# Kernel optimization log

Hardware: AMD Instinct MI355X
Metric: run time of the kernel (lower is better)

The kernel has to match this reference:

```python
import jax, jax.numpy as jnp
import numpy as np

B, S, V, P = 16, 100, 50000, 45
WE, PE, H = 100, 50, 400
H2 = 2 * H  # bilstm output size


def _lstm(x, Wih, Whh, b):
    """Unidirectional LSTM over time. x: [B,S,D] -> h: [B,S,H]. PyTorch gate order i,f,g,o."""
    Hs = Whh.shape[1]
    def step(carry, xt):
        h, c = carry
        g = xt @ Wih.T + h @ Whh.T + b
        i, f, gg, o = jnp.split(g, 4, axis=-1)
        c = jax.nn.sigmoid(f) * c + jax.nn.sigmoid(i) * jnp.tanh(gg)
        h = jax.nn.sigmoid(o) * jnp.tanh(c)
        return (h, c), h
    Bn = x.shape[0]
    init = (jnp.zeros((Bn, Hs), x.dtype), jnp.zeros((Bn, Hs), x.dtype))
    _, hs = jax.lax.scan(step, init, jnp.swapaxes(x, 0, 1))
    return jnp.swapaxes(hs, 0, 1)


def _bilstm_layer(x, Wf_ih, Wf_hh, bf, Wb_ih, Wb_hh, bb):
    hf = _lstm(x, Wf_ih, Wf_hh, bf)
    hb = _lstm(x[:, ::-1, :], Wb_ih, Wb_hh, bb)[:, ::-1, :]
    return jnp.concatenate([hf, hb], axis=-1)


def setup_inputs() -> dict:
    key = jax.random.key(0)
    ks = jax.random.split(key, 24)
    def n(k, shape, s=0.1):
        return jax.random.normal(k, shape, jnp.float32) * s
    inp = {
        "input_tokens": jax.random.randint(ks[0], (B, S), 0, V),
        "input_pos": jax.random.randint(ks[1], (B, S), 0, P),
        "input_head": jax.random.randint(ks[2], (B, S), 0, S),
        "word_W": n(ks[3], (V, WE)),
        "pos_W": n(ks[4], (P, PE)),
        "l0f_Wih": n(ks[5], (4 * H, WE + PE)), "l0f_Whh": n(ks[6], (4 * H, H)), "l0f_b": n(ks[7], (4 * H,)),
        "l0b_Wih": n(ks[8], (4 * H, WE + PE)), "l0b_Whh": n(ks[9], (4 * H, H)), "l0b_b": n(ks[10], (4 * H,)),
        "l1f_Wih": n(ks[11], (4 * H, H2)), "l1f_Whh": n(ks[12], (4 * H, H)), "l1f_b": n(ks[13], (4 * H,)),
        "l1b_Wih": n(ks[14], (4 * H, H2)), "l1b_Whh": n(ks[15], (4 * H, H)), "l1b_b": n(ks[16], (4 * H,)),
        "ua_W": n(ks[17], (H2, H2)), "ua_b": n(ks[18], (H2,)),
        "wa_W": n(ks[19], (H2, H2)), "wa_b": n(ks[20], (H2,)),
        "va_W": n(ks[21], (H2,)),
    }
    return inp


def reference(input_tokens, input_pos, input_head, word_W, pos_W,
              l0f_Wih, l0f_Whh, l0f_b, l0b_Wih, l0b_Whh, l0b_b,
              l1f_Wih, l1f_Whh, l1f_b, l1b_Wih, l1b_Whh, l1b_b,
              ua_W, ua_b, wa_W, wa_b, va_W):
    # embeddings (dropout is identity at eval)
    x = jnp.concatenate([word_W[input_tokens], pos_W[input_pos]], axis=-1)  # [B,S,150]
    h1 = _bilstm_layer(x, l0f_Wih, l0f_Whh, l0f_b, l0b_Wih, l0b_Whh, l0b_b)   # [B,S,H2]
    out = _bilstm_layer(h1, l1f_Wih, l1f_Whh, l1f_b, l1b_Wih, l1b_Whh, l1b_b)  # [B,S,H2]

    # batched additive biaffine scoring for targets i = 1..S-1 over all source positions j
    ua = out @ ua_W.T + ua_b  # u_a(source)  [B,S,H2]
    wa = out @ wa_W.T + wa_b  # w_a(target)  [B,S,H2]
    # g[b,t,j] = v_a . tanh(ua[b,j] + wa[b,t+1])
    g = jnp.einsum('btjh,h->btj', jnp.tanh(ua[:, None, :, :] + wa[:, 1:, None, :]), va_W)  # [B,S-1,S]
    # mask: output[:, j, 0] == output[:, i, 0]  (masks self, matching torch's output.eq(target)[:,:,0])
    mask = out[:, 1:, 0][:, :, None] == out[:, :, 0][:, None, :]  # [B,S-1,S]
    g = jnp.where(mask, -10000.0, g)
    logp = jax.nn.log_softmax(g, axis=2)  # log_softmax over source positions (torch dim=1)

    # loss: sum over i of NLLLoss(mean over batch, ignore_index=-1)
    gold = input_head[:, 1:]  # [B,S-1]
    valid = (gold != -1)
    nll = -jnp.take_along_axis(logp, jnp.clip(gold, 0, S - 1)[:, :, None], axis=2)[..., 0]
    nll = nll * valid.astype(logp.dtype)
    denom = jnp.maximum(valid.sum(axis=0), 1).astype(logp.dtype)
    loss = jnp.sum(nll.sum(axis=0) / denom)

    parent_prob_table = jnp.exp(logp)  # [B,S-1,S]
    preds = jnp.argmax(parent_prob_table, axis=2)  # [B,S-1]
    return (loss, preds, parent_prob_table)
```

## Files before the change

### kernel.cpp

```cpp
#include <hip/hip_runtime.h>

#define BB 16
#define SS 100
#define HH 400
#define H2 800
#define G4 1600
#define DIN0 150
#define KP0 160

#define OFF_GF   240000ULL
#define OFF_GB   2800000ULL
#define OFF_H1   5360000ULL
#define OFF_OUT2 6640000ULL
#define OFF_SC   7920000ULL
#define OFF_NLL  8078400ULL
#define OFF_EXH  8081600ULL
#define EX_U16_PER_PLANE 1331200ULL

#define PAD_X0   0ULL
#define PAD_WF   256000ULL
#define PAD_WB   512000ULL

typedef _Float16 f16x8 __attribute__((ext_vector_type(8)));
typedef float    f32x4 __attribute__((ext_vector_type(4)));
typedef unsigned long long u64x2 __attribute__((ext_vector_type(2)));

static __device__ __forceinline__ unsigned chkp(unsigned long long q) {
    return ((unsigned)q == 0xFFFFFFFFu) | ((unsigned)(q >> 32) == 0xFFFFFFFFu);
}
static __device__ __forceinline__ unsigned long long sanq(unsigned long long q) {
    if ((unsigned)q == 0xFFFFFFFFu)         q &= 0xFFFFFFFF00000000ull;
    if ((unsigned)(q >> 32) == 0xFFFFFFFFu) q &= 0x00000000FFFFFFFFull;
    return q;
}

__global__ __launch_bounds__(256) void embed_pad_kernel(
    const int* __restrict__ tok, const int* __restrict__ pos,
    const float* __restrict__ wW, const float* __restrict__ pW,
    const float* __restrict__ Wf, const float* __restrict__ Wb,
    float* __restrict__ stage)
{
    int idx = blockIdx.x * 256 + threadIdx.x;
    if (idx >= 3 * 1600 * KP0) return;
    int which = idx / (1600 * KP0);
    int rem = idx % (1600 * KP0);
    int r = rem / KP0, k = rem % KP0;
    float v = 0.f;
    if (which == 0) {
        if (k < 100)       v = wW[tok[r] * 100 + k];
        else if (k < 150)  v = pW[pos[r] * 50 + (k - 100)];
        stage[PAD_X0 + (size_t)r * KP0 + k] = v;
    } else if (which == 1) {
        if (k < DIN0) v = Wf[r * DIN0 + k];
        stage[PAD_WF + (size_t)r * KP0 + k] = v;
    } else {
        if (k < DIN0) v = Wb[r * DIN0 + k];
        stage[PAD_WB + (size_t)r * KP0 + k] = v;
    }
}

static __device__ __forceinline__ void cvt_pair8(float4 a, float4 b,
                                                 f16x8& hi, f16x8& lo)
{
    float v[8] = {a.x, a.y, a.z, a.w, b.x, b.y, b.z, b.w};
#pragma unroll
    for (int i = 0; i < 8; i++) {
        _Float16 h = (_Float16)v[i];
        hi[i] = h;
        lo[i] = (_Float16)((v[i] - (float)h) * 2048.f);
    }
}

__global__ __launch_bounds__(256) void gemm_nt_mfma_dual(
    const float* __restrict__ A,
    const float* __restrict__ W0, const float* __restrict__ b0, float* __restrict__ C0,
    const float* __restrict__ W1, const float* __restrict__ b1, float* __restrict__ C1,
    int N, int K, int R,
    unsigned int* __restrict__ poison, int poison_words)
{
    if (poison) {
        int nthreads = gridDim.x * gridDim.y * 256;
        int gtid = (blockIdx.y * gridDim.x + blockIdx.x) * 256 + threadIdx.x;
        for (int i = gtid; i < poison_words; i += nthreads) poison[i] = 0xFFFFFFFFu;
    }

    int half = gridDim.x >> 1;
    int sel = blockIdx.x >= half;
    int bx = blockIdx.x - (sel ? half : 0);
    const float* W = sel ? W1 : W0;
    const float* bias = sel ? b1 : b0;
    float* C = sel ? C1 : C0;

    int tid = threadIdx.x;
    int wv = tid >> 6, l = tid & 63;
    int lm = l & 15, lk = l >> 4;
    int rs = bx * 64 + wv * 16;
    if (rs >= R) return;
    int n0 = blockIdx.y * 64;

    const float* wrow = W + (size_t)(rs + lm) * K + lk * 8;
    const float* arow = A + (size_t)(n0 + lm) * K + lk * 8;

    f32x4 accH[4], accX[4];
#pragma unroll
    for (int ct = 0; ct < 4; ct++) {
        accH[ct] = {0.f, 0.f, 0.f, 0.f};
        accX[ct] = {0.f, 0.f, 0.f, 0.f};
    }

    int ksteps = K >> 5;
    for (int kt = 0; kt < ksteps; kt++) {
        int kb = kt << 5;
        float4 wlo4 = *(const float4*)(wrow + kb);
        float4 whi4 = *(const float4*)(wrow + kb + 4);
        f16x8 wh, wl;
        cvt_pair8(wlo4, whi4, wh, wl);
#pragma unroll
        for (int ct = 0; ct < 4; ct++) {
            const float* ap = arow + (size_t)(ct * 16) * K + kb;
            float4 aa = *(const float4*)ap;
            float4 ab = *(const float4*)(ap + 4);
            f16x8 ah, al;
            cvt_pair8(aa, ab, ah, al);
            accH[ct] = __builtin_amdgcn_mfma_f32_16x16x32_f16(wh, ah, accH[ct], 0, 0, 0);
            accX[ct] = __builtin_amdgcn_mfma_f32_16x16x32_f16(wh, al, accX[ct], 0, 0, 0);
            accX[ct] = __builtin_amdgcn_mfma_f32_16x16x32_f16(wl, ah, accX[ct], 0, 0, 0);
        }
    }

    float4 bv = *(const float4*)&bias[rs + lk * 4];
#pragma unroll
    for (int ct = 0; ct < 4; ct++) {
        f32x4 v = accH[ct] + accX[ct] * (1.f / 2048.f);
        float4 o;
        o.x = v[0] + bv.x; o.y = v[1] + bv.y; o.z = v[2] + bv.z; o.w = v[3] + bv.w;
        *(float4*)&C[(size_t)(n0 + ct * 16 + lm) * R + rs + lk * 4] = o;
    }
}

__global__ __launch_bounds__(64, 1) void lstm_layer_kernel(
    const float* __restrict__ Gf, const float* __restrict__ Gb,
    const float* __restrict__ Wf, const float* __restrict__ Wb,
    float* __restrict__ hbuf,
    unsigned short* __restrict__ exhi,
    unsigned short* __restrict__ exlo)
{
    const int dir = blockIdx.x / 100;
    const int wg  = blockIdx.x % 100;
    const int j0  = wg * 4;
    const float* __restrict__ G = dir ? Gb : Gf;
    const float* __restrict__ W = dir ? Wb : Wf;

    const int l   = threadIdx.x;
    const int b   = l & 15;
    const int hi4 = l >> 4;

    __shared__ __attribute__((aligned(16))) unsigned short ahi[13 * 64 * 8];
    __shared__ __attribute__((aligned(16))) unsigned short alo[13 * 64 * 8];
    __shared__ float gl[16 * 17];

    {
        const int m = b;
        const int g = m >> 2, jj = m & 3;
        const float* wrow = W + (size_t)(g * HH + j0 + jj) * HH;
        for (int kt = 0; kt < 13; kt++) {
            for (int e = 0; e < 8; e++) {
                int k = kt * 32 + hi4 * 8 + e;
                float w = (k < HH) ? wrow[k] : 0.f;
                _Float16 wh = (_Float16)w;
                _Float16 wl = (_Float16)((w - (float)wh) * 2048.f);
                ahi[(kt * 64 + l) * 8 + e] = __builtin_bit_cast(unsigned short, wh);
                alo[(kt * 64 + l) * 8 + e] = __builtin_bit_cast(unsigned short, wl);
            }
        }
    }
    __syncthreads();

    float c_reg = 0.f;
    unsigned short* exh_d = exhi + (size_t)dir * 100 * 13 * 512;
    unsigned short* exl_d = exlo + (size_t)dir * 100 * 13 * 512;
    const int pad_lane = (hi4 >= 2);

    for (int s = 0; s < SS; s++) {
        const int time = dir ? (SS - 1 - s) : s;
        f32x4 gpre = *(const f32x4*)&G[(size_t)(b * SS + time) * G4 + hi4 * HH + j0];

        f32x4 acc;
        if (s > 0) {
            const unsigned long long* pbh =
                (const unsigned long long*)(exh_d + (size_t)(s - 1) * 13 * 512);
            const unsigned long long* pbl =
                (const unsigned long long*)(exl_d + (size_t)(s - 1) * 13 * 512);
            u64x2 vh2[13], vl2[13];
            vh2[12] = {0ull, 0ull};
            vl2[12] = {0ull, 0ull};
            unsigned bad = 1;
            for (int guard = 0; guard < (1 << 13); guard++) {
                bad = 0;
#pragma unroll
                for (int kt = 0; kt < 12; kt++) {
                    size_t q = (size_t)(kt * 64 + l) * 2;
                    vh2[kt][0] = __hip_atomic_load(pbh + q,     __ATOMIC_RELAXED, __HIP_MEMORY_SCOPE_AGENT);
                    vh2[kt][1] = __hip_atomic_load(pbh + q + 1, __ATOMIC_RELAXED, __HIP_MEMORY_SCOPE_AGENT);
                    vl2[kt][0] = __hip_atomic_load(pbl + q,     __ATOMIC_RELAXED, __HIP_MEMORY_SCOPE_AGENT);
                    vl2[kt][1] = __hip_atomic_load(pbl + q + 1, __ATOMIC_RELAXED, __HIP_MEMORY_SCOPE_AGENT);
                }
                if (!pad_lane) {
                    size_t q = (size_t)(12 * 64 + l) * 2;
                    vh2[12][0] = __hip_atomic_load(pbh + q,     __ATOMIC_RELAXED, __HIP_MEMORY_SCOPE_AGENT);
                    vh2[12][1] = __hip_atomic_load(pbh + q + 1, __ATOMIC_RELAXED, __HIP_MEMORY_SCOPE_AGENT);
                    vl2[12][0] = __hip_atomic_load(pbl + q,     __ATOMIC_RELAXED, __HIP_MEMORY_SCOPE_AGENT);
                    vl2[12][1] = __hip_atomic_load(pbl + q + 1, __ATOMIC_RELAXED, __HIP_MEMORY_SCOPE_AGENT);
                    bad |= chkp(vh2[12][0]) | chkp(vh2[12][1])
                         | chkp(vl2[12][0]) | chkp(vl2[12][1]);
                }
#pragma unroll
                for (int kt = 0; kt < 12; kt++) {
                    bad |= chkp(vh2[kt][0]) | chkp(vh2[kt][1])
                         | chkp(vl2[kt][0]) | chkp(vl2[kt][1]);
                }
                if (__ballot(bad != 0) == 0ull) break;
                __builtin_amdgcn_s_sleep(2);
            }
            if (bad) {
#pragma unroll
                for (int kt = 0; kt < 13; kt++) {
                    vh2[kt][0] = sanq(vh2[kt][0]); vh2[kt][1] = sanq(vh2[kt][1]);
                    vl2[kt][0] = sanq(vl2[kt][0]); vl2[kt][1] = sanq(vl2[kt][1]);
                }
            }
            asm volatile("" ::: "memory");

            f32x4 aHH = gpre;
            f32x4 aHL = {0.f, 0.f, 0.f, 0.f};
            f32x4 aLH = {0.f, 0.f, 0.f, 0.f};
#pragma unroll
            for (int kt = 0; kt < 13; kt++) {
                f16x8 bhv = __builtin_bit_cast(f16x8, vh2[kt]);
                f16x8 blv = __builtin_bit_cast(f16x8, vl2[kt]);
                f16x8 wh = *(const f16x8*)&ahi[(kt * 64 + l) * 8];
                f16x8 wl = *(const f16x8*)&alo[(kt * 64 + l) * 8];
                aHH = __builtin_amdgcn_mfma_f32_16x16x32_f16(wh, bhv, aHH, 0, 0, 0);
                aHL = __builtin_amdgcn_mfma_f32_16x16x32_f16(wh, blv, aHL, 0, 0, 0);
                aLH = __builtin_amdgcn_mfma_f32_16x16x32_f16(wl, bhv, aLH, 0, 0, 0);
            }
            acc = aHH + (aHL + aLH) * (1.f / 2048.f);
        } else {
            acc = gpre;
        }

#pragma unroll
        for (int q = 0; q < 4; q++) gl[(4 * hi4 + q) * 17 + b] = acc[q];
        __syncthreads();

        const int jj = hi4;
        float gi = gl[( 0 + jj) * 17 + b];
        float gf = gl[( 4 + jj) * 17 + b];
        float gg = gl[( 8 + jj) * 17 + b];
        float go = gl[(12 + jj) * 17 + b];
        __syncthreads();

        float si = 1.f / (1.f + expf(-gi));
        float sf = 1.f / (1.f + expf(-gf));
        float tg = tanhf(gg);
        float so = 1.f / (1.f + expf(-go));
        float c  = sf * c_reg + si * tg;
        c_reg = c;
        float h  = so * tanhf(c);

        if (s < SS - 1) {
            _Float16 hh = (_Float16)h;
            _Float16 hl = (_Float16)((h - (float)hh) * 2048.f);
            unsigned uh = __builtin_bit_cast(unsigned short, hh);
            unsigned ul = __builtin_bit_cast(unsigned short, hl);
            unsigned ph = uh | (((unsigned)__shfl_down((int)uh, 16)) << 16);
            unsigned pl = ul | (((unsigned)__shfl_down((int)ul, 16)) << 16);
            if ((jj & 1) == 0) {
                int k0 = j0 + jj;
                int kt = k0 >> 5, ko = k0 & 31;
                int lg = ko >> 3, e = ko & 7;
                size_t u16idx = ((size_t)(s * 13 + kt) * 64 + (lg * 16 + b)) * 8 + e;
                __hip_atomic_store((unsigned*)(exh_d + u16idx), ph,
                                   __ATOMIC_RELAXED, __HIP_MEMORY_SCOPE_AGENT);
                __hip_atomic_store((unsigned*)(exl_d + u16idx), pl,
                                   __ATOMIC_RELAXED, __HIP_MEMORY_SCOPE_AGENT);
            }
        }

        hbuf[(size_t)(b * SS + time) * H2 + dir * HH + j0 + jj] = h;
    }
}

#define ITILE 11
__global__ __launch_bounds__(256) void attn_scores_kernel(
    const float* __restrict__ ua, const float* __restrict__ wa,
    const float* __restrict__ va, float* __restrict__ scores)
{
    int b  = blockIdx.x / 9;
    int i0 = (blockIdx.x % 9) * ITILE;
    int tid = threadIdx.x;
    __shared__ float ua_t[100][101];
    __shared__ float wa_t[ITILE][102];
    __shared__ float sacc[ITILE][101];
    __shared__ float va_t[100];

    for (int p = tid; p < ITILE * 101; p += 256) ((float*)sacc)[p] = 0.f;

    for (int ht = 0; ht < 8; ht++) {
        int h0 = ht * 100;
        __syncthreads();
        for (int p = tid; p < 100 * 100; p += 256) {
            int j = p / 100, hh = p % 100;
            ua_t[j][hh] = ua[(size_t)(b * SS + j) * H2 + h0 + hh];
        }
        for (int p = tid; p < ITILE * 100; p += 256) {
            int il = p / 100, hh = p % 100;
            wa_t[il][hh] = wa[(size_t)(b * SS + i0 + il + 1) * H2 + h0 + hh];
        }
        if (tid < 100) va_t[tid] = va[h0 + tid];
        __syncthreads();
        for (int p = tid; p < ITILE * 100; p += 256) {
            int il = p / 100, j = p % 100;
            float acc = 0.f;
#pragma unroll 4
            for (int hh = 0; hh < 100; hh++) {
                float x = ua_t[j][hh] + wa_t[il][hh];
                float z = __expf(2.f * x);
                float th = 1.f - 2.f * __builtin_amdgcn_rcpf(z + 1.f);
                acc = fmaf(th, va_t[hh], acc);
            }
            sacc[il][j] += acc;
        }
    }
    __syncthreads();
    for (int p = tid; p < ITILE * 100; p += 256) {
        int il = p / 100, j = p % 100;
        scores[(size_t)(b * 99 + i0 + il) * 100 + j] = sacc[il][j];
    }
}

__global__ __launch_bounds__(128) void attn_softmax_kernel(
    const float* __restrict__ scores, const float* __restrict__ out2,
    const int* __restrict__ head, float* __restrict__ outb,
    float* __restrict__ nll)
{
    int bi = blockIdx.x;
    int b = bi / 99, i = bi % 99;
    int j = threadIdx.x;
    __shared__ float sv[128];
    __shared__ int   si[128];
    __shared__ float red[128];

    float h_t = out2[(size_t)(b * SS + i + 1) * H2];
    float sj = -1e30f;
    if (j < 100) {
        sj = scores[(size_t)bi * 100 + j];
        float h_j = out2[(size_t)(b * SS + j) * H2];
        if (h_j == h_t) sj = -10000.0f;
    }
    sv[j] = sj; si[j] = j;
    __syncthreads();
    for (int off = 64; off >= 1; off >>= 1) {
        if (j < off) {
            float o = sv[j + off]; int oi = si[j + off];
            if (o > sv[j] || (o == sv[j] && oi < si[j])) { sv[j] = o; si[j] = oi; }
        }
        __syncthreads();
    }
    float m = sv[0]; int amax = si[0];
    __syncthreads();
    float e = (j < 100) ? __expf(sj - m) : 0.f;
    red[j] = e;
    __syncthreads();
    for (int off = 64; off >= 1; off >>= 1) {
        if (j < off) red[j] += red[j + off];
        __syncthreads();
    }
    float sum = red[0];
    float inv = 1.f / sum;
    if (j < 100) outb[1 + 1584 + (size_t)bi * 100 + j] = e * inv;
    if (j == 0) {
        outb[1 + bi] = (float)amax;
        int gold = head[b * SS + i + 1];
        bool valid = (gold != -1);
        int gc = gold < 0 ? 0 : (gold > 99 ? 99 : gold);
        float sgc = scores[(size_t)bi * 100 + gc];
        float hgc = out2[(size_t)(b * SS + gc) * H2];
        if (hgc == h_t) sgc = -10000.0f;
        nll[bi] = valid ? -(sgc - m - logf(sum)) : 0.f;
    }
}

__global__ __launch_bounds__(128) void loss_kernel(
    const float* __restrict__ nll, const int* __restrict__ head,
    float* __restrict__ outb)
{
    __shared__ float red[128];
    int tid = threadIdx.x;
    float contrib = 0.f;
    if (tid < 99) {
        int i = tid;
        float tot = 0.f; int cv = 0;
        for (int b = 0; b < BB; b++) {
            tot += nll[b * 99 + i];
            cv += (head[b * SS + i + 1] != -1) ? 1 : 0;
        }
        int denom = cv > 0 ? cv : 1;
        contrib = tot / (float)denom;
    }
    red[tid] = contrib;
    __syncthreads();
    for (int off = 64; off >= 1; off >>= 1) {
        if (tid < off) red[tid] += red[tid + off];
        __syncthreads();
    }
    if (tid == 0) outb[0] = red[0];
}

extern "C" void kernel_launch(void* const* d_in, const int* in_sizes, int n_in,
                              void* d_out, int out_size, void* d_ws, size_t ws_size,
                              hipStream_t stream) {
    const int*   tok     = (const int*)d_in[0];
    const int*   pos     = (const int*)d_in[1];
    const int*   head    = (const int*)d_in[2];
    const float* word_W  = (const float*)d_in[3];
    const float* pos_W   = (const float*)d_in[4];
    const float* l0f_Wih = (const float*)d_in[5];
    const float* l0f_Whh = (const float*)d_in[6];
    const float* l0f_b   = (const float*)d_in[7];
    const float* l0b_Wih = (const float*)d_in[8];
    const float* l0b_Whh = (const float*)d_in[9];
    const float* l0b_b   = (const float*)d_in[10];
    const float* l1f_Wih = (const float*)d_in[11];
    const float* l1f_Whh = (const float*)d_in[12];
    const float* l1f_b   = (const float*)d_in[13];
    const float* l1b_Wih = (const float*)d_in[14];
    const float* l1b_Whh = (const float*)d_in[15];
    const float* l1b_b   = (const float*)d_in[16];
    const float* ua_W    = (const float*)d_in[17];
    const float* ua_b    = (const float*)d_in[18];
    const float* wa_W    = (const float*)d_in[19];
    const float* wa_b    = (const float*)d_in[20];
    const float* va_W    = (const float*)d_in[21];

    float* ws   = (float*)d_ws;
    float* gf   = ws + OFF_GF;
    float* gb   = ws + OFF_GB;
    float* h1   = ws + OFF_H1;
    float* out2 = ws + OFF_OUT2;
    float* sc   = ws + OFF_SC;
    float* nllb = ws + OFF_NLL;
    unsigned short* exhi = (unsigned short*)(ws + OFF_EXH);
    unsigned short* exlo = exhi + EX_U16_PER_PLANE;
    float* outf = (float*)d_out;

    hipMemsetAsync(exhi, 0xFF, 2 * EX_U16_PER_PLANE * sizeof(unsigned short), stream);

    embed_pad_kernel<<<dim3((3 * 1600 * KP0 + 255) / 256), 256, 0, stream>>>(
        tok, pos, word_W, pos_W, l0f_Wih, l0b_Wih, out2);

    float* x0p = out2 + PAD_X0;
    float* wfp = out2 + PAD_WF;
    float* wbp = out2 + PAD_WB;

    gemm_nt_mfma_dual<<<dim3(50, 25), 256, 0, stream>>>(
        x0p, wfp, l0f_b, gf, wbp, l0b_b, gb, 1600, KP0, G4, nullptr, 0);
    lstm_layer_kernel<<<dim3(200), 64, 0, stream>>>(
        gf, gb, l0f_Whh, l0b_Whh, h1, exhi, exlo);
    gemm_nt_mfma_dual<<<dim3(50, 25), 256, 0, stream>>>(
        h1, l1f_Wih, l1f_b, gf, l1b_Wih, l1b_b, gb, 1600, H2, G4,
        (unsigned int*)exhi, (int)EX_U16_PER_PLANE);
    lstm_layer_kernel<<<dim3(200), 64, 0, stream>>>(
        gf, gb, l1f_Whh, l1b_Whh, out2, exhi, exlo);
    gemm_nt_mfma_dual<<<dim3(26, 25), 256, 0, stream>>>(
        out2, ua_W, ua_b, gf, wa_W, wa_b, gb, 1600, H2, H2, nullptr, 0);
    attn_scores_kernel<<<dim3(16 * 9), 256, 0, stream>>>(gf, gb, va_W, sc);
    attn_softmax_kernel<<<dim3(1584), 128, 0, stream>>>(sc, out2, head, outf, nllb);
    loss_kernel<<<dim3(1), 128, 0, stream>>>(nllb, head, outf);
}
```

Before: 1.440 ms.

## Fuse embedding gather into layer-0 GEMM and softmax into attention scores

The embedding and weight padding kernel and the memset are replaced by a layer-0 GEMM that gathers word and position embeddings directly, masks K beyond 150, and poisons the exchange buffer itself. The attention scores kernel now performs the masking, softmax, argmax and NLL from shared memory using wave shuffles, so the separate softmax kernel and the scores buffer round trip go away. This cuts two launches and several global round trips. The cost is uncoalesced per-lane gathers inside the GEMM inner loop and fewer blocks available for the softmax work.

```diff
diff --git a/kernel.cpp b/kernel.cpp
--- a/kernel.cpp
+++ b/kernel.cpp
@@ -12,14 +12,9 @@
 #define OFF_GB   2800000ULL
 #define OFF_H1   5360000ULL
 #define OFF_OUT2 6640000ULL
-#define OFF_SC   7920000ULL
 #define OFF_NLL  8078400ULL
 #define OFF_EXH  8081600ULL
 #define EX_U16_PER_PLANE 1331200ULL
-
-#define PAD_X0   0ULL
-#define PAD_WF   256000ULL
-#define PAD_WB   512000ULL
 
 typedef _Float16 f16x8 __attribute__((ext_vector_type(8)));
 typedef float    f32x4 __attribute__((ext_vector_type(4)));
@@ -34,40 +29,101 @@
     return q;
 }
 
-__global__ __launch_bounds__(256) void embed_pad_kernel(
-    const int* __restrict__ tok, const int* __restrict__ pos,
-    const float* __restrict__ wW, const float* __restrict__ pW,
-    const float* __restrict__ Wf, const float* __restrict__ Wb,
-    float* __restrict__ stage)
-{
-    int idx = blockIdx.x * 256 + threadIdx.x;
-    if (idx >= 3 * 1600 * KP0) return;
-    int which = idx / (1600 * KP0);
-    int rem = idx % (1600 * KP0);
-    int r = rem / KP0, k = rem % KP0;
-    float v = 0.f;
-    if (which == 0) {
-        if (k < 100)       v = wW[tok[r] * 100 + k];
-        else if (k < 150)  v = pW[pos[r] * 50 + (k - 100)];
-        stage[PAD_X0 + (size_t)r * KP0 + k] = v;
-    } else if (which == 1) {
-        if (k < DIN0) v = Wf[r * DIN0 + k];
-        stage[PAD_WF + (size_t)r * KP0 + k] = v;
-    } else {
-        if (k < DIN0) v = Wb[r * DIN0 + k];
-        stage[PAD_WB + (size_t)r * KP0 + k] = v;
-    }
-}
-
-static __device__ __forceinline__ void cvt_pair8(float4 a, float4 b,
-                                                 f16x8& hi, f16x8& lo)
-{
-    float v[8] = {a.x, a.y, a.z, a.w, b.x, b.y, b.z, b.w};
+static __device__ __forceinline__ void cvt8(const float* v, f16x8& hi, f16x8& lo)
+{
 #pragma unroll
     for (int i = 0; i < 8; i++) {
         _Float16 h = (_Float16)v[i];
         hi[i] = h;
         lo[i] = (_Float16)((v[i] - (float)h) * 2048.f);
+    }
+}
+static __device__ __forceinline__ void cvt_pair8(float4 a, float4 b,
+                                                 f16x8& hi, f16x8& lo)
+{
+    float v[8] = {a.x, a.y, a.z, a.w, b.x, b.y, b.z, b.w};
+    cvt8(v, hi, lo);
+}
+
+__global__ __launch_bounds__(256) void gemm_l0_embed_dual(
+    const int* __restrict__ tok, const int* __restrict__ pos,
+    const float* __restrict__ wW, const float* __restrict__ pW,
+    const float* __restrict__ W0, const float* __restrict__ b0, float* __restrict__ C0,
+    const float* __restrict__ W1, const float* __restrict__ b1, float* __restrict__ C1,
+    unsigned int* __restrict__ poison, int poison_words)
+{
+    {
+        int nthreads = gridDim.x * gridDim.y * 256;
+        int gtid = (blockIdx.y * gridDim.x + blockIdx.x) * 256 + threadIdx.x;
+        for (int i = gtid; i < poison_words; i += nthreads) poison[i] = 0xFFFFFFFFu;
+    }
+
+    int half = gridDim.x >> 1;
+    int sel = blockIdx.x >= half;
+    int bx = blockIdx.x - (sel ? half : 0);
+    const float* W = sel ? W1 : W0;
+    const float* bias = sel ? b1 : b0;
+    float* C = sel ? C1 : C0;
+
+    int tid = threadIdx.x;
+    int wv = tid >> 6, l = tid & 63;
+    int lm = l & 15, lk = l >> 4;
+    int rs = bx * 64 + wv * 16;
+    int n0 = blockIdx.y * 64;
+
+    int trow[4], prow[4];
+#pragma unroll
+    for (int ct = 0; ct < 4; ct++) {
+        int r = n0 + ct * 16 + lm;
+        trow[ct] = tok[r];
+        prow[ct] = pos[r];
+    }
+    const float* wrow = W + (size_t)(rs + lm) * DIN0;
+
+    f32x4 accH[4], accX[4];
+#pragma unroll
+    for (int ct = 0; ct < 4; ct++) {
+        accH[ct] = {0.f, 0.f, 0.f, 0.f};
+        accX[ct] = {0.f, 0.f, 0.f, 0.f};
+    }
+
+#pragma unroll
+    for (int kt = 0; kt < 5; kt++) {
+        int kb = kt << 5;
+        float wv8[8];
+#pragma unroll
+        for (int e = 0; e < 8; e++) {
+            int k = kb + lk * 8 + e;
+            wv8[e] = (k < DIN0) ? wrow[k] : 0.f;
+        }
+        f16x8 wh, wl;
+        cvt8(wv8, wh, wl);
+#pragma unroll
+        for (int ct = 0; ct < 4; ct++) {
+            float av8[8];
+#pragma unroll
+            for (int e = 0; e < 8; e++) {
+                int k = kb + lk * 8 + e;
+                float v = 0.f;
+                if (k < 100)       v = wW[trow[ct] * 100 + k];
+                else if (k < DIN0) v = pW[prow[ct] * 50 + (k - 100)];
+                av8[e] = v;
+            }
+            f16x8 ah, al;
+            cvt8(av8, ah, al);
+            accH[ct] = __builtin_amdgcn_mfma_f32_16x16x32_f16(wh, ah, accH[ct], 0, 0, 0);
+            accX[ct] = __builtin_amdgcn_mfma_f32_16x16x32_f16(wh, al, accX[ct], 0, 0, 0);
+            accX[ct] = __builtin_amdgcn_mfma_f32_16x16x32_f16(wl, ah, accX[ct], 0, 0, 0);
+        }
+    }
+
+    float4 bv = *(const float4*)&bias[rs + lk * 4];
+#pragma unroll
+    for (int ct = 0; ct < 4; ct++) {
+        f32x4 v = accH[ct] + accX[ct] * (1.f / 2048.f);
+        float4 o;
+        o.x = v[0] + bv.x; o.y = v[1] + bv.y; o.z = v[2] + bv.z; o.w = v[3] + bv.w;
+        *(float4*)&C[(size_t)(n0 + ct * 16 + lm) * G4 + rs + lk * 4] = o;
     }
 }
 
@@ -292,9 +348,11 @@
 }
 
 #define ITILE 11
-__global__ __launch_bounds__(256) void attn_scores_kernel(
+__global__ __launch_bounds__(256) void attn_scores_softmax_kernel(
     const float* __restrict__ ua, const float* __restrict__ wa,
-    const float* __restrict__ va, float* __restrict__ scores)
+    const float* __restrict__ va, const float* __restrict__ out2,
+    const int* __restrict__ head, float* __restrict__ outb,
+    float* __restrict__ nll)
 {
     int b  = blockIdx.x / 9;
     int i0 = (blockIdx.x % 9) * ITILE;
@@ -303,21 +361,23 @@
     __shared__ float wa_t[ITILE][102];
     __shared__ float sacc[ITILE][101];
     __shared__ float va_t[100];
+    __shared__ float h0[100];
 
     for (int p = tid; p < ITILE * 101; p += 256) ((float*)sacc)[p] = 0.f;
+    if (tid < 100) h0[tid] = out2[(size_t)(b * SS + tid) * H2];
 
     for (int ht = 0; ht < 8; ht++) {
-        int h0 = ht * 100;
+        int hh0 = ht * 100;
         __syncthreads();
         for (int p = tid; p < 100 * 100; p += 256) {
             int j = p / 100, hh = p % 100;
-            ua_t[j][hh] = ua[(size_t)(b * SS + j) * H2 + h0 + hh];
+            ua_t[j][hh] = ua[(size_t)(b * SS + j) * H2 + hh0 + hh];
         }
         for (int p = tid; p < ITILE * 100; p += 256) {
             int il = p / 100, hh = p % 100;
-            wa_t[il][hh] = wa[(size_t)(b * SS + i0 + il + 1) * H2 + h0 + hh];
-        }
-        if (tid < 100) va_t[tid] = va[h0 + tid];
+            wa_t[il][hh] = wa[(size_t)(b * SS + i0 + il + 1) * H2 + hh0 + hh];
+        }
+        if (tid < 100) va_t[tid] = va[hh0 + tid];
         __syncthreads();
         for (int p = tid; p < ITILE * 100; p += 256) {
             int il = p / 100, j = p % 100;
@@ -333,61 +393,44 @@
         }
     }
     __syncthreads();
-    for (int p = tid; p < ITILE * 100; p += 256) {
-        int il = p / 100, j = p % 100;
-        scores[(size_t)(b * 99 + i0 + il) * 100 + j] = sacc[il][j];
-    }
-}
-
-__global__ __launch_bounds__(128) void attn_softmax_kernel(
-    const float* __restrict__ scores, const float* __restrict__ out2,
-    const int* __restrict__ head, float* __restrict__ outb,
-    float* __restrict__ nll)
-{
-    int bi = blockIdx.x;
-    int b = bi / 99, i = bi % 99;
-    int j = threadIdx.x;
-    __shared__ float sv[128];
-    __shared__ int   si[128];
-    __shared__ float red[128];
-
-    float h_t = out2[(size_t)(b * SS + i + 1) * H2];
-    float sj = -1e30f;
-    if (j < 100) {
-        sj = scores[(size_t)bi * 100 + j];
-        float h_j = out2[(size_t)(b * SS + j) * H2];
-        if (h_j == h_t) sj = -10000.0f;
-    }
-    sv[j] = sj; si[j] = j;
-    __syncthreads();
-    for (int off = 64; off >= 1; off >>= 1) {
-        if (j < off) {
-            float o = sv[j + off]; int oi = si[j + off];
-            if (o > sv[j] || (o == sv[j] && oi < si[j])) { sv[j] = o; si[j] = oi; }
-        }
-        __syncthreads();
-    }
-    float m = sv[0]; int amax = si[0];
-    __syncthreads();
-    float e = (j < 100) ? __expf(sj - m) : 0.f;
-    red[j] = e;
-    __syncthreads();
-    for (int off = 64; off >= 1; off >>= 1) {
-        if (j < off) red[j] += red[j + off];
-        __syncthreads();
-    }
-    float sum = red[0];
-    float inv = 1.f / sum;
-    if (j < 100) outb[1 + 1584 + (size_t)bi * 100 + j] = e * inv;
-    if (j == 0) {
-        outb[1 + bi] = (float)amax;
-        int gold = head[b * SS + i + 1];
-        bool valid = (gold != -1);
-        int gc = gold < 0 ? 0 : (gold > 99 ? 99 : gold);
-        float sgc = scores[(size_t)bi * 100 + gc];
-        float hgc = out2[(size_t)(b * SS + gc) * H2];
-        if (hgc == h_t) sgc = -10000.0f;
-        nll[bi] = valid ? -(sgc - m - logf(sum)) : 0.f;
+
+    int wv = tid >> 6, ln = tid & 63;
+    for (int il = wv; il < ITILE; il += 4) {
+        int i = i0 + il;
+        int bi = b * 99 + i;
+        float h_t = h0[i + 1];
+        int j1 = ln, j2 = ln + 64;
+        float s1 = sacc[il][j1];
+        if (h0[j1] == h_t) s1 = -10000.0f;
+        float s2 = -1e30f;
+        if (j2 < 100) {
+            s2 = sacc[il][j2];
+            if (h0[j2] == h_t) s2 = -10000.0f;
+        }
+        float v = s1; int vi = j1;
+        if (s2 > v) { v = s2; vi = j2; }
+        for (int k = 32; k >= 1; k >>= 1) {
+            float vo = __shfl_xor(v, k);
+            int   io = __shfl_xor(vi, k);
+            if (vo > v || (vo == v && io < vi)) { v = vo; vi = io; }
+        }
+        float m = v; int amax = vi;
+        float e1 = __expf(s1 - m);
+        float e2 = (j2 < 100) ? __expf(s2 - m) : 0.f;
+        float sum = e1 + e2;
+        for (int k = 32; k >= 1; k >>= 1) sum += __shfl_xor(sum, k);
+        float inv = 1.f / sum;
+        outb[1 + 1584 + (size_t)bi * 100 + j1] = e1 * inv;
+        if (j2 < 100) outb[1 + 1584 + (size_t)bi * 100 + j2] = e2 * inv;
+        if (ln == 0) {
+            outb[1 + bi] = (float)amax;
+            int gold = head[b * SS + i + 1];
+            bool valid = (gold != -1);
+            int gc = gold < 0 ? 0 : (gold > 99 ? 99 : gold);
+            float sgc = sacc[il][gc];
+            if (h0[gc] == h_t) sgc = -10000.0f;
+            nll[bi] = valid ? -(sgc - m - logf(sum)) : 0.f;
+        }
     }
 }
 
@@ -448,23 +491,15 @@
     float* gb   = ws + OFF_GB;
     float* h1   = ws + OFF_H1;
     float* out2 = ws + OFF_OUT2;
-    float* sc   = ws + OFF_SC;
     float* nllb = ws + OFF_NLL;
     unsigned short* exhi = (unsigned short*)(ws + OFF_EXH);
     unsigned short* exlo = exhi + EX_U16_PER_PLANE;
     float* outf = (float*)d_out;
 
-    hipMemsetAsync(exhi, 0xFF, 2 * EX_U16_PER_PLANE * sizeof(unsigned short), stream);
-
-    embed_pad_kernel<<<dim3((3 * 1600 * KP0 + 255) / 256), 256, 0, stream>>>(
-        tok, pos, word_W, pos_W, l0f_Wih, l0b_Wih, out2);
-
-    float* x0p = out2 + PAD_X0;
-    float* wfp = out2 + PAD_WF;
-    float* wbp = out2 + PAD_WB;
-
-    gemm_nt_mfma_dual<<<dim3(50, 25), 256, 0, stream>>>(
-        x0p, wfp, l0f_b, gf, wbp, l0b_b, gb, 1600, KP0, G4, nullptr, 0);
+    gemm_l0_embed_dual<<<dim3(50, 25), 256, 0, stream>>>(
+        tok, pos, word_W, pos_W,
+        l0f_Wih, l0f_b, gf, l0b_Wih, l0b_b, gb,
+        (unsigned int*)exhi, (int)EX_U16_PER_PLANE);
     lstm_layer_kernel<<<dim3(200), 64, 0, stream>>>(
         gf, gb, l0f_Whh, l0b_Whh, h1, exhi, exlo);
     gemm_nt_mfma_dual<<<dim3(50, 25), 256, 0, stream>>>(
@@ -474,7 +509,7 @@
         gf, gb, l1f_Whh, l1b_Whh, out2, exhi, exlo);
     gemm_nt_mfma_dual<<<dim3(26, 25), 256, 0, stream>>>(
         out2, ua_W, ua_b, gf, wa_W, wa_b, gb, 1600, H2, H2, nullptr, 0);
-    attn_scores_kernel<<<dim3(16 * 9), 256, 0, stream>>>(gf, gb, va_W, sc);
-    attn_softmax_kernel<<<dim3(1584), 128, 0, stream>>>(sc, out2, head, outf, nllb);
+    attn_scores_softmax_kernel<<<dim3(16 * 9), 256, 0, stream>>>(
+        gf, gb, va_W, out2, head, outf, nllb);
     loss_kernel<<<dim3(1), 128, 0, stream>>>(nllb, head, outf);
 }
```

New measurement: 1.435 ms. Within noise of the previous version (-0.3%).
